# Kernel optimization log

Measured on AMD Instinct MI355X. Metric: run time of the kernel, lower is better.

## Reference

```python
import jax, jax.numpy as jnp
import numpy as np

DIM = 1024
B, N = 8, 4096
EPS = 1e-6


def setup_inputs() -> dict:
    key = jax.random.key(0)
    k1, k2, k3, k4 = jax.random.split(key, 4)
    x = jax.random.normal(k1, (B, N, DIM), dtype=jnp.float32)
    # torch nn.Linear weights: W_qkv [3*dim, dim], W_out [dim, dim], b_out [dim]
    s = 1.0 / np.sqrt(DIM)
    W_qkv = jax.random.uniform(k2, (3 * DIM, DIM), jnp.float32, -s, s)
    W_out = jax.random.uniform(k3, (DIM, DIM), jnp.float32, -s, s)
    b_out = jax.random.uniform(k4, (DIM,), jnp.float32, -s, s)
    return {"x": x, "W_qkv": W_qkv, "W_out": W_out, "b_out": b_out}


def reference(x, W_qkv, W_out, b_out):
    # qkv projection (Linear without bias): x @ W_qkv.T -> [B,N,3D]
    qkv = jnp.einsum('bnd,ed->bne', x, W_qkv)
    q, k, v = jnp.split(qkv, 3, axis=-1)
    q = jax.nn.relu(q) + EPS
    k = jax.nn.relu(k) + EPS
    # kv accumulation: [B,D,D]
    kv = jnp.einsum('bnd,bne->bde', k, v)
    # normalizer z: [B,N]
    z = 1.0 / (jnp.einsum('bnd,bd->bn', q, k.sum(axis=1)) + EPS)
    # attn output: [B,N,D]
    attn = jnp.einsum('bnd,bde,bn->bne', q, kv, z)
    # output projection with bias
    return jnp.einsum('bne,fe->bnf', attn, W_out) + b_out
```

## Files before the change

kernel.cpp:

```cpp
#include <hip/hip_runtime.h>


#define EPS 1e-6f

using u16 = unsigned short;
typedef __attribute__((ext_vector_type(4))) float f32x4;
typedef __attribute__((ext_vector_type(8))) __bf16 bf16x8;

__device__ __forceinline__ u16 f2b(float f) {
  unsigned u = __builtin_bit_cast(unsigned, f);
  u += 0x7FFFu + ((u >> 16) & 1u);
  return (u16)(u >> 16);
}
__device__ __forceinline__ float b2f(u16 h) {
  return __builtin_bit_cast(float, (unsigned)h << 16);
}

typedef const __attribute__((address_space(1))) void* gas1_t;
typedef __attribute__((address_space(3))) void* las3_t;

__device__ __forceinline__ void load16_to_lds(const void* g, void* l) {
  __builtin_amdgcn_global_load_lds((gas1_t)g, (las3_t)l, 16, 0, 0);
}

template<int MODE>
__global__ __launch_bounds__(256) void gemm_abT(
    const u16* __restrict__ A, const u16* __restrict__ B, void* __restrict__ Cv,
    int M, int N, int K, int lda, int ldb, int ldc,
    long long sA, long long sB, long long sC,
    const float* __restrict__ zvec, const float* __restrict__ bias,
    u16* __restrict__ kT, u16* __restrict__ vT, float* __restrict__ ksum)
{
  __shared__ u16 lA[128 * 32];
  __shared__ u16 lB[128 * 32];
  const int tid  = threadIdx.x;
  const int wave = tid >> 6, lane = tid & 63;
  const int TN = gridDim.y;
  const int lin = blockIdx.x + gridDim.x * blockIdx.y;
  const int xcd = lin & 7, g = lin >> 3;
  const int bm = (g / TN) * 8 + xcd;
  const int bn = g % TN;
  const int bz = blockIdx.z;
  const u16* Ab = A + (long long)bz * sA;
  const u16* Bb = B + (long long)bz * sB;

  const int c0 = wave * 64 + lane;
  const int c1 = 256 + c0;
  const u16* gA0 = Ab + (long long)(bm * 128 + (c0 >> 2)) * lda + (c0 & 3) * 8;
  const u16* gA1 = Ab + (long long)(bm * 128 + (c1 >> 2)) * lda + (c1 & 3) * 8;
  const u16* gB0 = Bb + (long long)(bn * 128 + (c0 >> 2)) * ldb + (c0 & 3) * 8;
  const u16* gB1 = Bb + (long long)(bn * 128 + (c1 >> 2)) * ldb + (c1 & 3) * 8;
  u16* lA0 = &lA[(wave * 64) * 8];
  u16* lA1 = &lA[(256 + wave * 64) * 8];
  u16* lB0 = &lB[(wave * 64) * 8];
  u16* lB1 = &lB[(256 + wave * 64) * 8];

  const int wm = (wave & 1) * 64, wn = (wave >> 1) * 64;
  const int aoff = (wm + (lane & 15)) * 32 + (lane >> 4) * 8;
  const int boff = (wn + (lane & 15)) * 32 + (lane >> 4) * 8;

  f32x4 acc[4][4];
  #pragma unroll
  for (int i = 0; i < 4; i++)
    #pragma unroll
    for (int j = 0; j < 4; j++) acc[i][j] = f32x4{0.f, 0.f, 0.f, 0.f};

  for (int k0 = 0; k0 < K; k0 += 32) {
    load16_to_lds(gA0 + k0, lA0);
    load16_to_lds(gA1 + k0, lA1);
    load16_to_lds(gB0 + k0, lB0);
    load16_to_lds(gB1 + k0, lB1);
    __syncthreads();
    bf16x8 af[4], bfv[4];
    #pragma unroll
    for (int i = 0; i < 4; i++) af[i]  = *(const bf16x8*)&lA[aoff + i * 16 * 32];
    #pragma unroll
    for (int j = 0; j < 4; j++) bfv[j] = *(const bf16x8*)&lB[boff + j * 16 * 32];
    #pragma unroll
    for (int i = 0; i < 4; i++)
      #pragma unroll
      for (int j = 0; j < 4; j++)
        acc[i][j] = __builtin_amdgcn_mfma_f32_16x16x32_bf16(af[i], bfv[j], acc[i][j], 0, 0, 0);
    __syncthreads();
  }

  const int quad = lane >> 4, lc = lane & 15;
  const int rowb = bm * 128 + wm + quad * 4;
  const int colb = bn * 128 + wn + lc;

  if (MODE == 0) {
    const int region = colb >> 10;
    if (region == 0) {
      u16* q = (u16*)Cv;
      #pragma unroll
      for (int i = 0; i < 4; i++)
        #pragma unroll
        for (int j = 0; j < 4; j++) {
          const int col = colb + j * 16;
          #pragma unroll
          for (int r = 0; r < 4; r++) {
            const int row = rowb + i * 16 + r;
            q[(long long)row * ldc + col] = f2b(fmaxf(acc[i][j][r], 0.f) + EPS);
          }
        }
    } else {
      const bool isk = (region == 1);
      const int b = rowb >> 12;
      u16* dst = (isk ? kT : vT) + (long long)b * 1024 * 4096;
      const int nloc = rowb & 4095;
      #pragma unroll
      for (int j = 0; j < 4; j++) {
        const int d = colb + j * 16 - region * 1024;
        float s = 0.f;
        #pragma unroll
        for (int i = 0; i < 4; i++) {
          ushort4 pk;
          #pragma unroll
          for (int r = 0; r < 4; r++) {
            float v = acc[i][j][r];
            if (isk) { v = fmaxf(v, 0.f) + EPS; s += v; }
            (&pk.x)[r] = f2b(v);
          }
          *(ushort4*)(dst + (long long)d * 4096 + nloc + i * 16) = pk;
        }
        if (isk) {
          s += __shfl_xor(s, 16);
          s += __shfl_xor(s, 32);
          if (quad == 0) atomicAdd(&ksum[b * 1024 + d], s);
        }
      }
    }
  } else {
    #pragma unroll
    for (int i = 0; i < 4; i++) {
      #pragma unroll
      for (int j = 0; j < 4; j++) {
        const int col = colb + j * 16;
        float bj = 0.f;
        if (MODE == 2) bj = bias[col];
        #pragma unroll
        for (int r = 0; r < 4; r++) {
          const int row = rowb + i * 16 + r;
          float v = acc[i][j][r];
          if (MODE == 1) {
            ((u16*)Cv + (long long)bz * sC)[(long long)row * ldc + col] = f2b(v);
          } else {
            float zz = zvec[(long long)bz * M + row];
            ((float*)Cv + (long long)bz * sC)[(long long)row * ldc + col] = v * zz + bj;
          }
        }
      }
    }
  }
}

__global__ void cvt_f32_bf16(const float* __restrict__ s, u16* __restrict__ d, int n4) {
  int i = blockIdx.x * blockDim.x + threadIdx.x;
  int st = gridDim.x * blockDim.x;
  for (; i < n4; i += st) {
    float4 f = ((const float4*)s)[i];
    uint2 o;
    o.x = (unsigned)f2b(f.x) | ((unsigned)f2b(f.y) << 16);
    o.y = (unsigned)f2b(f.z) | ((unsigned)f2b(f.w) << 16);
    ((uint2*)d)[i] = o;
  }
}

__global__ void zero_f32(float* __restrict__ p, int n) {
  int i = blockIdx.x * blockDim.x + threadIdx.x;
  if (i < n) p[i] = 0.f;
}

__global__ void z_kernel(const u16* __restrict__ qbuf, const float* __restrict__ ksum,
                         float* __restrict__ z) {
  const int row  = blockIdx.x * 4 + (threadIdx.x >> 6);
  const int lane = threadIdx.x & 63;
  const int b = row >> 12;
  const uint4* q = (const uint4*)(qbuf + (long long)row * 1024);
  const float* ks = ksum + b * 1024;
  float s = 0.f;
  #pragma unroll
  for (int c = 0; c < 2; c++) {
    int idx = lane + c * 64;
    uint4 d = q[idx];
    unsigned w[4] = {d.x, d.y, d.z, d.w};
    const float* kk = ks + idx * 8;
    #pragma unroll
    for (int qq = 0; qq < 4; qq++)
      s += b2f((u16)(w[qq] & 0xFFFF)) * kk[qq * 2]
         + b2f((u16)(w[qq] >> 16))    * kk[qq * 2 + 1];
  }
  #pragma unroll
  for (int o = 32; o > 0; o >>= 1) s += __shfl_down(s, o);
  if (lane == 0) z[row] = 1.0f / (s + EPS);
}

extern "C" void kernel_launch(void* const* d_in, const int* in_sizes, int n_in,
                              void* d_out, int out_size, void* d_ws, size_t ws_size,
                              hipStream_t stream) {
  const float* x    = (const float*)d_in[0];
  const float* Wqkv = (const float*)d_in[1];
  const float* Wout = (const float*)d_in[2];
  const float* bout = (const float*)d_in[3];

  char* ws = (char*)d_ws;
  u16* x_bf    = (u16*)(ws + 0);
  u16* qbuf    = (u16*)(ws + 67108864);
  u16* kT      = (u16*)(ws + 134217728);
  u16* vT      = (u16*)(ws + 201326592);
  u16* wqkv_bf = (u16*)(ws + 268435456);
  u16* wout_bf = (u16*)(ws + 274726912);
  u16* kv      = (u16*)(ws + 276824064);
  u16* kvwT    = (u16*)(ws + 293601280);
  float* ksum  = (float*)(ws + 310378496);
  float* z     = (float*)(ws + 310411264);

  cvt_f32_bf16<<<4096, 256, 0, stream>>>(x,    x_bf,    33554432 / 4);
  cvt_f32_bf16<<<1024, 256, 0, stream>>>(Wqkv, wqkv_bf,  3145728 / 4);
  cvt_f32_bf16<<<512,  256, 0, stream>>>(Wout, wout_bf,  1048576 / 4);
  zero_f32<<<32, 256, 0, stream>>>(ksum, 8192);

  gemm_abT<0><<<dim3(256, 24, 1), 256, 0, stream>>>(
      x_bf, wqkv_bf, qbuf, 32768, 3072, 1024, 1024, 1024, 1024,
      0, 0, 0, nullptr, nullptr, kT, vT, ksum);

  z_kernel<<<8192, 256, 0, stream>>>(qbuf, ksum, z);

  gemm_abT<1><<<dim3(8, 8, 8), 256, 0, stream>>>(
      kT, vT, kv, 1024, 1024, 4096, 4096, 4096, 1024,
      4194304, 4194304, 1048576, nullptr, nullptr, nullptr, nullptr, nullptr);

  gemm_abT<1><<<dim3(8, 8, 8), 256, 0, stream>>>(
      wout_bf, kv, kvwT, 1024, 1024, 1024, 1024, 1024, 1024,
      0, 1048576, 1048576, nullptr, nullptr, nullptr, nullptr, nullptr);

  gemm_abT<2><<<dim3(32, 8, 8), 256, 0, stream>>>(
      qbuf, kvwT, d_out, 4096, 1024, 1024, 1024, 1024, 1024,
      4194304, 1048576, 4194304, z, bout, nullptr, nullptr, nullptr);
}
```

Before: 793.6 us.

## Add 256x256 double-buffered swizzled GEMM kernel for QKV and output projections

Adds a new 512-thread GEMM kernel with 256x256 output tiles, a 64-wide K step, double-buffered LDS staging through global_load_lds, XOR-swizzled LDS layout, and interleaved load/MFMA phases with setprio. The kernel replaces the 128x128 single-buffered GEMM for the large QKV projection and the final output projection. The goal is more data reuse per tile, fewer LDS bank conflicts, and overlap of global loads with MFMA work. In exchange it uses 128KB of LDS per block and heavier register pressure, and the tail grids are smaller, which may hurt occupancy.

```diff
diff --git a/kernel.cpp b/kernel.cpp
--- a/kernel.cpp
+++ b/kernel.cpp
@@ -21,6 +21,226 @@
 
 __device__ __forceinline__ void load16_to_lds(const void* g, void* l) {
   __builtin_amdgcn_global_load_lds((gas1_t)g, (las3_t)l, 16, 0, 0);
+}
+
+#define BARRIER() do { asm volatile("" ::: "memory"); __builtin_amdgcn_s_barrier(); asm volatile("" ::: "memory"); } while (0)
+#define WAITL0()  asm volatile("s_waitcnt lgkmcnt(0)" ::: "memory")
+#define WAITV(n)  asm volatile("s_waitcnt vmcnt(" #n ")" ::: "memory")
+#define MFMA16(a, b, c) __builtin_amdgcn_mfma_f32_16x16x32_bf16((a), (b), (c), 0, 0, 0)
+
+__device__ __forceinline__ void stage_half(const u16* g, int ld, u16* l,
+                                           int r0, int csw, int woff) {
+  load16_to_lds(g + (long long)r0 * ld + csw, l + woff);
+  load16_to_lds(g + (long long)(r0 + 64) * ld + csw, l + 4096 + woff);
+}
+
+template<int MODE>
+__global__ __launch_bounds__(512, 2) void gemm256(
+    const u16* __restrict__ A, const u16* __restrict__ B, void* __restrict__ Cv,
+    int M, int N, int K, int lda, int ldb, int ldc,
+    long long sA, long long sB, long long sC,
+    const float* __restrict__ zvec, const float* __restrict__ bias,
+    u16* __restrict__ kT, u16* __restrict__ vT, float* __restrict__ ksum)
+{
+  __shared__ __align__(16) u16 shA[32768];
+  __shared__ __align__(16) u16 shB[32768];
+
+  const int tid  = threadIdx.x;
+  const int lane = tid & 63, wave = tid >> 6;
+  const int wr = wave >> 2, wc = wave & 3;
+  const int quad = lane >> 4, lc = lane & 15;
+
+  const int TN = gridDim.y;
+  const int lin = blockIdx.x + gridDim.x * blockIdx.y;
+  const int xcd = lin & 7, g = lin >> 3;
+  const int bm = (g / TN) * 8 + xcd;
+  const int bn = g % TN;
+  const int bz = blockIdx.z;
+  const u16* Ab = A + (long long)bz * sA;
+  const u16* Bb = B + (long long)bz * sB;
+
+  const int r0   = tid >> 3;
+  const int csw  = (((tid & 7) ^ ((tid >> 3) & 7)) << 3);
+  const int woff = wave * 512;
+
+  const int ch0 = ((quad ^ (lane & 7)) << 3);
+  const int ch1 = (((4 + quad) ^ (lane & 7)) << 3);
+  const int aRow = wr * 128 + lc;
+  const int bRow = wc * 64 + lc;
+
+  const int NT = K >> 6;
+
+  f32x4 acc[8][4];
+  #pragma unroll
+  for (int i = 0; i < 8; ++i)
+    #pragma unroll
+    for (int j = 0; j < 4; ++j) acc[i][j] = f32x4{0.f, 0.f, 0.f, 0.f};
+
+  auto stA = [&](int h, int t) {
+    stage_half(Ab + ((long long)bm * 256 + h * 128) * lda + t * 64, lda,
+               shA + (t & 1) * 16384 + h * 8192, r0, csw, woff);
+  };
+  auto stB = [&](int h, int t) {
+    stage_half(Bb + ((long long)bn * 256 + h * 128) * ldb + t * 64, ldb,
+               shB + (t & 1) * 16384 + h * 8192, r0, csw, woff);
+  };
+
+  stA(0, 0); stA(1, 0); stB(0, 0); stB(1, 0);
+  if (NT > 1) { stA(0, 1); stA(1, 1); stB(0, 1); WAITV(6); }
+  else        { WAITV(0); }
+  BARRIER();
+
+  for (int t = 0; t < NT; ++t) {
+    const u16* aB = shA + (t & 1) * 16384;
+    const u16* bB = shB + (t & 1) * 16384;
+    bf16x8 aF[4][2], b01[2][2], b23[2][2];
+
+    #pragma unroll
+    for (int i = 0; i < 4; ++i) {
+      aF[i][0] = *(const bf16x8*)&aB[(aRow + i * 16) * 64 + ch0];
+      aF[i][1] = *(const bf16x8*)&aB[(aRow + i * 16) * 64 + ch1];
+    }
+    #pragma unroll
+    for (int j = 0; j < 2; ++j) {
+      b01[j][0] = *(const bf16x8*)&bB[(bRow + j * 16) * 64 + ch0];
+      b01[j][1] = *(const bf16x8*)&bB[(bRow + j * 16) * 64 + ch1];
+    }
+    if (t + 1 < NT) stB(1, t + 1);
+    BARRIER(); WAITL0();
+    __builtin_amdgcn_s_setprio(1);
+    #pragma unroll
+    for (int i = 0; i < 4; ++i)
+      #pragma unroll
+      for (int j = 0; j < 2; ++j) {
+        acc[i][j] = MFMA16(aF[i][0], b01[j][0], acc[i][j]);
+        acc[i][j] = MFMA16(aF[i][1], b01[j][1], acc[i][j]);
+      }
+    __builtin_amdgcn_s_setprio(0);
+    BARRIER();
+
+    #pragma unroll
+    for (int j = 0; j < 2; ++j) {
+      b23[j][0] = *(const bf16x8*)&bB[(bRow + (2 + j) * 16) * 64 + ch0];
+      b23[j][1] = *(const bf16x8*)&bB[(bRow + (2 + j) * 16) * 64 + ch1];
+    }
+    BARRIER(); WAITL0();
+    __builtin_amdgcn_s_setprio(1);
+    #pragma unroll
+    for (int i = 0; i < 4; ++i)
+      #pragma unroll
+      for (int j = 0; j < 2; ++j) {
+        acc[i][2 + j] = MFMA16(aF[i][0], b23[j][0], acc[i][2 + j]);
+        acc[i][2 + j] = MFMA16(aF[i][1], b23[j][1], acc[i][2 + j]);
+      }
+    __builtin_amdgcn_s_setprio(0);
+    BARRIER();
+
+    #pragma unroll
+    for (int i = 0; i < 4; ++i) {
+      aF[i][0] = *(const bf16x8*)&aB[(aRow + (4 + i) * 16) * 64 + ch0];
+      aF[i][1] = *(const bf16x8*)&aB[(aRow + (4 + i) * 16) * 64 + ch1];
+    }
+    if (t + 2 < NT) stB(0, t + 2);
+    BARRIER(); WAITL0();
+    __builtin_amdgcn_s_setprio(1);
+    #pragma unroll
+    for (int i = 0; i < 4; ++i)
+      #pragma unroll
+      for (int j = 0; j < 2; ++j) {
+        acc[4 + i][j] = MFMA16(aF[i][0], b01[j][0], acc[4 + i][j]);
+        acc[4 + i][j] = MFMA16(aF[i][1], b01[j][1], acc[4 + i][j]);
+      }
+    __builtin_amdgcn_s_setprio(0);
+    BARRIER();
+
+    if (t + 2 < NT) { stA(0, t + 2); stA(1, t + 2); }
+    BARRIER(); WAITL0();
+    __builtin_amdgcn_s_setprio(1);
+    #pragma unroll
+    for (int i = 0; i < 4; ++i)
+      #pragma unroll
+      for (int j = 0; j < 2; ++j) {
+        acc[4 + i][2 + j] = MFMA16(aF[i][0], b23[j][0], acc[4 + i][2 + j]);
+        acc[4 + i][2 + j] = MFMA16(aF[i][1], b23[j][1], acc[4 + i][2 + j]);
+      }
+    __builtin_amdgcn_s_setprio(0);
+    if (t + 2 < NT) { WAITV(6); } else { WAITV(0); }
+    BARRIER();
+  }
+
+  const long long rowb = (long long)bm * 256 + wr * 128 + quad * 4;
+  const int colb = bn * 256 + wc * 64 + lc;
+
+  if (MODE == 0) {
+    const int region = colb >> 10;
+    if (region == 0) {
+      u16* q = (u16*)Cv;
+      #pragma unroll
+      for (int i = 0; i < 8; ++i)
+        #pragma unroll
+        for (int j = 0; j < 4; ++j) {
+          const int col = colb + j * 16;
+          #pragma unroll
+          for (int r = 0; r < 4; ++r) {
+            const long long row = rowb + i * 16 + r;
+            q[row * ldc + col] = f2b(fmaxf(acc[i][j][r], 0.f) + EPS);
+          }
+        }
+    } else {
+      const bool isk = (region == 1);
+      const int b = (int)(rowb >> 12);
+      u16* dst = (isk ? kT : vT) + (long long)b * 1024 * 4096;
+      const int nloc = (int)(rowb & 4095);
+      #pragma unroll
+      for (int j = 0; j < 4; ++j) {
+        const int d = colb + j * 16 - region * 1024;
+        float s = 0.f;
+        #pragma unroll
+        for (int i = 0; i < 8; ++i) {
+          ushort4 pk;
+          #pragma unroll
+          for (int r = 0; r < 4; ++r) {
+            float v = acc[i][j][r];
+            if (isk) { v = fmaxf(v, 0.f) + EPS; s += v; }
+            (&pk.x)[r] = f2b(v);
+          }
+          *(ushort4*)(dst + (long long)d * 4096 + nloc + i * 16) = pk;
+        }
+        if (isk) {
+          s += __shfl_xor(s, 16);
+          s += __shfl_xor(s, 32);
+          if (quad == 0) atomicAdd(&ksum[b * 1024 + d], s);
+        }
+      }
+    }
+  } else if (MODE == 2) {
+    float* out = (float*)Cv + (long long)bz * sC;
+    #pragma unroll
+    for (int i = 0; i < 8; ++i)
+      #pragma unroll
+      for (int j = 0; j < 4; ++j) {
+        const int col = colb + j * 16;
+        const float bj = bias[col];
+        #pragma unroll
+        for (int r = 0; r < 4; ++r) {
+          const long long row = rowb + i * 16 + r;
+          out[row * ldc + col] = acc[i][j][r] * zvec[(long long)bz * M + row] + bj;
+        }
+      }
+  } else {
+    u16* out = (u16*)Cv + (long long)bz * sC;
+    #pragma unroll
+    for (int i = 0; i < 8; ++i)
+      #pragma unroll
+      for (int j = 0; j < 4; ++j) {
+        const int col = colb + j * 16;
+        #pragma unroll
+        for (int r = 0; r < 4; ++r) {
+          const long long row = rowb + i * 16 + r;
+          out[row * ldc + col] = f2b(acc[i][j][r]);
+        }
+      }
+  }
 }
 
 template<int MODE>
@@ -80,7 +300,7 @@
     for (int i = 0; i < 4; i++)
       #pragma unroll
       for (int j = 0; j < 4; j++)
-        acc[i][j] = __builtin_amdgcn_mfma_f32_16x16x32_bf16(af[i], bfv[j], acc[i][j], 0, 0, 0);
+        acc[i][j] = MFMA16(af[i], bfv[j], acc[i][j]);
     __syncthreads();
   }
 
@@ -88,70 +308,27 @@
   const int rowb = bm * 128 + wm + quad * 4;
   const int colb = bn * 128 + wn + lc;
 
-  if (MODE == 0) {
-    const int region = colb >> 10;
-    if (region == 0) {
-      u16* q = (u16*)Cv;
-      #pragma unroll
-      for (int i = 0; i < 4; i++)
-        #pragma unroll
-        for (int j = 0; j < 4; j++) {
-          const int col = colb + j * 16;
-          #pragma unroll
-          for (int r = 0; r < 4; r++) {
-            const int row = rowb + i * 16 + r;
-            q[(long long)row * ldc + col] = f2b(fmaxf(acc[i][j][r], 0.f) + EPS);
-          }
-        }
-    } else {
-      const bool isk = (region == 1);
-      const int b = rowb >> 12;
-      u16* dst = (isk ? kT : vT) + (long long)b * 1024 * 4096;
-      const int nloc = rowb & 4095;
-      #pragma unroll
-      for (int j = 0; j < 4; j++) {
-        const int d = colb + j * 16 - region * 1024;
-        float s = 0.f;
-        #pragma unroll
-        for (int i = 0; i < 4; i++) {
-          ushort4 pk;
-          #pragma unroll
-          for (int r = 0; r < 4; r++) {
-            float v = acc[i][j][r];
-            if (isk) { v = fmaxf(v, 0.f) + EPS; s += v; }
-            (&pk.x)[r] = f2b(v);
-          }
-          *(ushort4*)(dst + (long long)d * 4096 + nloc + i * 16) = pk;
-        }
-        if (isk) {
-          s += __shfl_xor(s, 16);
-          s += __shfl_xor(s, 32);
-          if (quad == 0) atomicAdd(&ksum[b * 1024 + d], s);
-        }
-      }
-    }
-  } else {
-    #pragma unroll
-    for (int i = 0; i < 4; i++) {
-      #pragma unroll
-      for (int j = 0; j < 4; j++) {
-        const int col = colb + j * 16;
-        float bj = 0.f;
-        if (MODE == 2) bj = bias[col];
-        #pragma unroll
-        for (int r = 0; r < 4; r++) {
-          const int row = rowb + i * 16 + r;
-          float v = acc[i][j][r];
-          if (MODE == 1) {
-            ((u16*)Cv + (long long)bz * sC)[(long long)row * ldc + col] = f2b(v);
-          } else {
-            float zz = zvec[(long long)bz * M + row];
-            ((float*)Cv + (long long)bz * sC)[(long long)row * ldc + col] = v * zz + bj;
-          }
-        }
-      }
-    }
-  }
+  #pragma unroll
+  for (int i = 0; i < 4; i++) {
+    #pragma unroll
+    for (int j = 0; j < 4; j++) {
+      const int col = colb + j * 16;
+      float bj = 0.f;
+      if (MODE == 2) bj = bias[col];
+      #pragma unroll
+      for (int r = 0; r < 4; r++) {
+        const int row = rowb + i * 16 + r;
+        float v = acc[i][j][r];
+        if (MODE == 1) {
+          ((u16*)Cv + (long long)bz * sC)[(long long)row * ldc + col] = f2b(v);
+        } else if (MODE == 2) {
+          float zz = zvec[(long long)bz * M + row];
+          ((float*)Cv + (long long)bz * sC)[(long long)row * ldc + col] = v * zz + bj;
+        }
+      }
+    }
+  }
+  (void)kT; (void)vT; (void)ksum;
 }
 
 __global__ void cvt_f32_bf16(const float* __restrict__ s, u16* __restrict__ d, int n4) {
@@ -220,7 +397,7 @@
   cvt_f32_bf16<<<512,  256, 0, stream>>>(Wout, wout_bf,  1048576 / 4);
   zero_f32<<<32, 256, 0, stream>>>(ksum, 8192);
 
-  gemm_abT<0><<<dim3(256, 24, 1), 256, 0, stream>>>(
+  gemm256<0><<<dim3(128, 12, 1), 512, 0, stream>>>(
       x_bf, wqkv_bf, qbuf, 32768, 3072, 1024, 1024, 1024, 1024,
       0, 0, 0, nullptr, nullptr, kT, vT, ksum);
 
@@ -234,7 +411,7 @@
       wout_bf, kv, kvwT, 1024, 1024, 1024, 1024, 1024, 1024,
       0, 1048576, 1048576, nullptr, nullptr, nullptr, nullptr, nullptr);
 
-  gemm_abT<2><<<dim3(32, 8, 8), 256, 0, stream>>>(
+  gemm256<2><<<dim3(16, 4, 8), 512, 0, stream>>>(
       qbuf, kvwT, d_out, 4096, 1024, 1024, 1024, 1024, 1024,
       4194304, 1048576, 4194304, z, bout, nullptr, nullptr, nullptr);
 }
```

New measurement: 708.6 us. 1.12x faster.
